# Kernel optimization log

Measured on AMD Instinct MI355X. Metric: run time of the kernel, lower is better.

## Reference

```python
import jax, jax.numpy as jnp
import numpy as np

L, B, S, CACHE = 2, 1, 2048, 2048
H, HKV, D, DM, FF, V = 16, 8, 128, 2048, 8192, 32000
EPS = 1e-6
ROPE_BASE = 10000.0


def setup_inputs() -> dict:
    key = jax.random.key(0)
    ks = jax.random.split(key, 18)
    std = 0.02
    r = lambda k, shape: (jax.random.normal(k, shape, dtype=jnp.float32) * std)
    return {
        "input_ids": jax.random.randint(ks[0], (B, S), 0, V),
        "embed": r(ks[1], (V, DM)),
        "Wq": r(ks[2], (L, DM, H * D)),
        "Wk": r(ks[3], (L, DM, HKV * D)),
        "Wv": r(ks[4], (L, DM, HKV * D)),
        "Wo": r(ks[5], (L, H * D, DM)),
        "Wg": r(ks[6], (L, DM, FF)),
        "Wu": r(ks[7], (L, DM, FF)),
        "Wd": r(ks[8], (L, FF, DM)),
        "ln1": jnp.ones((L, DM), jnp.float32),
        "ln2": jnp.ones((L, DM), jnp.float32),
        "final_norm": jnp.ones((DM,), jnp.float32),
        "lm_head": r(ks[9], (DM, V)),
        "k_cache": jax.random.normal(ks[10], (L, B, H, CACHE, D), jnp.float32),
        "v_cache": jax.random.normal(ks[11], (L, B, H, CACHE, D), jnp.float32),
    }


def rms_norm(x, w):
    return x * jax.lax.rsqrt(jnp.mean(x * x, axis=-1, keepdims=True) + EPS) * w


def apply_rope(x, pos):
    # x: [B,H,T,D], pos: [T]
    inv_freq = 1.0 / (ROPE_BASE ** (jnp.arange(0, D, 2, dtype=jnp.float32) / D))
    f = pos[:, None].astype(jnp.float32) * inv_freq[None, :]  # [T, D/2]
    emb = jnp.concatenate([f, f], axis=-1)                    # [T, D]
    cos, sin = jnp.cos(emb), jnp.sin(emb)
    rot = jnp.concatenate([-x[..., D // 2:], x[..., : D // 2]], axis=-1)
    return x * cos + rot * sin


def decoder_forward(input_ids, embed, Wq, Wk, Wv, Wo, Wg, Wu, Wd,
                    ln1, ln2, final_norm, lm_head, k_cache, v_cache):
    h = embed[input_ids]  # [B,S,DM]
    T = CACHE + S
    q_pos = jnp.arange(CACHE, CACHE + S)
    k_pos = jnp.arange(T)
    # causal mask: query i (global pos CACHE+i) attends keys <= CACHE+i
    mask = k_pos[None, :] <= (CACHE + jnp.arange(S))[:, None]  # [S,T]
    scale = 1.0 / np.sqrt(D)

    def layer(h, params):
        wq, wk, wv, wo, wg, wu, wd, l1, l2, kc, vc = params
        x = rms_norm(h, l1)
        q = (x @ wq).reshape(B, S, H, D).transpose(0, 2, 1, 3)     # [B,H,S,D]
        k = (x @ wk).reshape(B, S, HKV, D).transpose(0, 2, 1, 3)   # [B,HKV,S,D]
        v = (x @ wv).reshape(B, S, HKV, D).transpose(0, 2, 1, 3)
        k = jnp.repeat(k, H // HKV, axis=1)                        # repeat_kv
        v = jnp.repeat(v, H // HKV, axis=1)
        k = jnp.concatenate([kc, k], axis=2)                       # [B,H,T,D]
        v = jnp.concatenate([vc, v], axis=2)
        q = apply_rope(q, q_pos)
        k = apply_rope(k, k_pos)
        scores = jnp.einsum('bhqd,bhkd->bhqk', q, k) * scale
        scores = jnp.where(mask, scores, jnp.float32(-1e30))
        attn = jax.nn.softmax(scores, axis=-1)
        o = jnp.einsum('bhqk,bhkd->bhqd', attn, v)
        o = o.transpose(0, 2, 1, 3).reshape(B, S, H * D) @ wo
        h = h + o
        x = rms_norm(h, l2)
        h = h + (jax.nn.silu(x @ wg) * (x @ wu)) @ wd
        return h, None

    h, _ = jax.lax.scan(layer, h, (Wq, Wk, Wv, Wo, Wg, Wu, Wd, ln1, ln2, k_cache, v_cache))
    h = rms_norm(h, final_norm)
    return (h @ lm_head).astype(jnp.float32)  # logits [B,S,V]


def reference(input_ids, embed, Wq, Wk, Wv, Wo, Wg, Wu, Wd,
              ln1, ln2, final_norm, lm_head, k_cache, v_cache):
    return decoder_forward(input_ids, embed, Wq, Wk, Wv, Wo, Wg, Wu, Wd,
                           ln1, ln2, final_norm, lm_head, k_cache, v_cache)
```

## Files before the change

### kernel.cpp

```cpp
#include <hip/hip_runtime.h>

typedef __attribute__((ext_vector_type(8))) short bfrag8;
typedef __attribute__((ext_vector_type(4))) short bfrag4;
typedef __attribute__((ext_vector_type(4))) float facc4;

#define DEV_INLINE __device__ __forceinline__

DEV_INLINE short f2bf(float f) {
    union { float f; unsigned u; } x; x.f = f;
    unsigned r = (x.u + 0x7FFFu + ((x.u >> 16) & 1u)) >> 16;
    return (short)r;
}

DEV_INLINE unsigned pack_bf2(float a, float b) {
    return (unsigned)(unsigned short)f2bf(a) | ((unsigned)(unsigned short)f2bf(b) << 16);
}

#define GL2LDS(gp, lp) __builtin_amdgcn_global_load_lds( \
    (const __attribute__((address_space(1))) void*)(gp), \
    (__attribute__((address_space(3))) void*)(lp), 16, 0, 0)

#define MFMA16(a, b, c) __builtin_amdgcn_mfma_f32_16x16x32_bf16((a), (b), (c), 0, 0, 0)

__global__ __launch_bounds__(256) void embed_kernel(const int* __restrict__ ids,
                                                    const float* __restrict__ emb,
                                                    float* __restrict__ h) {
    int s = blockIdx.x;
    int id = ids[s];
    const float* src = emb + (size_t)id * 2048;
    float* dst = h + (size_t)s * 2048;
    int t = threadIdx.x;
    float4 a = *(const float4*)(src + t * 8);
    float4 b = *(const float4*)(src + t * 8 + 4);
    *(float4*)(dst + t * 8) = a;
    *(float4*)(dst + t * 8 + 4) = b;
}

__global__ __launch_bounds__(256) void rmsnorm_bf16_kernel(const float* __restrict__ in,
                                                           const float* __restrict__ w,
                                                           short* __restrict__ out) {
    int row = blockIdx.x;
    const float* x = in + (size_t)row * 2048;
    short* y = out + (size_t)row * 2048;
    int t = threadIdx.x;
    float4 a = *(const float4*)(x + t * 8);
    float4 b = *(const float4*)(x + t * 8 + 4);
    float ss = a.x*a.x + a.y*a.y + a.z*a.z + a.w*a.w
             + b.x*b.x + b.y*b.y + b.z*b.z + b.w*b.w;
#pragma unroll
    for (int off = 32; off >= 1; off >>= 1) ss += __shfl_xor(ss, off);
    __shared__ float red[4];
    if ((t & 63) == 0) red[t >> 6] = ss;
    __syncthreads();
    float tot = red[0] + red[1] + red[2] + red[3];
    float sc = rsqrtf(tot * (1.0f / 2048.0f) + 1e-6f);
    float4 wa = *(const float4*)(w + t * 8);
    float4 wb = *(const float4*)(w + t * 8 + 4);
    bfrag8 o;
    o[0] = f2bf(a.x * sc * wa.x); o[1] = f2bf(a.y * sc * wa.y);
    o[2] = f2bf(a.z * sc * wa.z); o[3] = f2bf(a.w * sc * wa.w);
    o[4] = f2bf(b.x * sc * wb.x); o[5] = f2bf(b.y * sc * wb.y);
    o[6] = f2bf(b.z * sc * wb.z); o[7] = f2bf(b.w * sc * wb.w);
    *(bfrag8*)(y + t * 8) = o;
}

__global__ __launch_bounds__(256) void wconv_kernel(const float* __restrict__ W,
                                                    short* __restrict__ Wt,
                                                    int K, int N) {
    __shared__ short Lt[64][72];
    int k0 = blockIdx.x * 64, n0 = blockIdx.y * 64;
    int tid = threadIdx.x;
    int r = tid >> 4, c = (tid & 15) * 4;
#pragma unroll
    for (int j = 0; j < 4; ++j) {
        int k = r + j * 16;
        float4 v = *(const float4*)(W + (size_t)(k0 + k) * N + n0 + c);
        Lt[c + 0][k] = f2bf(v.x); Lt[c + 1][k] = f2bf(v.y);
        Lt[c + 2][k] = f2bf(v.z); Lt[c + 3][k] = f2bf(v.w);
    }
    __syncthreads();
    int n = tid >> 3, kk = (tid & 7) * 8;
#pragma unroll
    for (int j = 0; j < 2; ++j)
        *(bfrag8*)(Wt + (size_t)(n0 + n + j * 32) * K + k0 + kk) = *(const bfrag8*)&Lt[n + j * 32][kk];
}

template<int BM, bool ADD>
__global__ __launch_bounds__(256) void gemm_bt(const short* __restrict__ A,
                                               const short* __restrict__ Bt,
                                               float* __restrict__ C,
                                               int K, int N) {
    __shared__ short As[BM * 32];
    __shared__ short Bs[128 * 32];
    constexpr int NW = (BM == 128) ? 4 : 2;
    int tid = threadIdx.x;
    int lane = tid & 63, wave = tid >> 6;

    int gx = gridDim.x;
    int nwg = gx * gridDim.y;
    int b = blockIdx.y * gx + blockIdx.x;
    int q = nwg >> 3, r8 = nwg & 7;
    int xcd = b & 7, idx = b >> 3;
    int lb = (xcd < r8) ? (xcd * (q + 1) + idx) : (r8 * (q + 1) + (xcd - r8) * q + idx);
    int bm = (lb % gx) * BM, bn = (lb / gx) * 128;

    int wr = (BM == 128) ? ((wave >> 1) * 64) : 0;
    int wc = (BM == 128) ? ((wave & 1) * 64) : (wave * 32);
    int lr = lane & 15, lg = lane >> 4;

    facc4 acc[4][NW];
#pragma unroll
    for (int m = 0; m < 4; ++m)
#pragma unroll
        for (int n = 0; n < NW; ++n) acc[m][n] = (facc4){0.f, 0.f, 0.f, 0.f};

    int stR = wave * 16 + (lane >> 2);
    int stK = (lane & 3) * 8;
    const short* Ag = A + (size_t)(bm + stR) * K + stK;
    const short* Bg = Bt + (size_t)(bn + stR) * K + stK;
    short* AsP = As + stR * 32 + stK;
    short* BsP = Bs + stR * 32 + stK;

    for (int k0 = 0; k0 < K; k0 += 32) {
        GL2LDS(Ag + k0, AsP);
        if (BM == 128) GL2LDS(Ag + (size_t)64 * K + k0, AsP + 64 * 32);
        GL2LDS(Bg + k0, BsP);
        GL2LDS(Bg + (size_t)64 * K + k0, BsP + 64 * 32);
        __syncthreads();
        bfrag8 a[4], bfr[NW];
#pragma unroll
        for (int m = 0; m < 4; ++m)
            a[m] = *(const bfrag8*)&As[(wr + m * 16 + lr) * 32 + lg * 8];
#pragma unroll
        for (int n = 0; n < NW; ++n)
            bfr[n] = *(const bfrag8*)&Bs[(wc + n * 16 + lr) * 32 + lg * 8];
#pragma unroll
        for (int m = 0; m < 4; ++m)
#pragma unroll
            for (int n = 0; n < NW; ++n)
                acc[m][n] = MFMA16(a[m], bfr[n], acc[m][n]);
        __syncthreads();
    }
#pragma unroll
    for (int m = 0; m < 4; ++m)
#pragma unroll
        for (int n = 0; n < NW; ++n)
#pragma unroll
            for (int r = 0; r < 4; ++r) {
                size_t ci = (size_t)(bm + wr + m * 16 + lg * 4 + r) * N + bn + wc + n * 16 + lr;
                C[ci] = ADD ? (C[ci] + acc[m][n][r]) : acc[m][n][r];
            }
}

__global__ __launch_bounds__(512, 2) void gemm8(const short* __restrict__ A,
                                                const short* __restrict__ Bt,
                                                float* __restrict__ C,
                                                int K, int N) {
    __shared__ short lds[65536];
    char* ldsb = (char*)lds;
    int tid = threadIdx.x;
    int lane = tid & 63, wave = tid >> 6;
    int wm = wave >> 2, wn = wave & 3;
    int lr = lane & 15, lg = lane >> 4;

    int gx = gridDim.x;
    int nwg = gx * gridDim.y;
    int b = blockIdx.y * gx + blockIdx.x;
    int q8 = nwg >> 3, r8 = nwg & 7;
    int xcd = b & 7, idx = b >> 3;
    int lb = (xcd < r8) ? (xcd * (q8 + 1) + idx) : (r8 * (q8 + 1) + (xcd - r8) * q8 + idx);
    int bm = (lb % gx) * 256, bn = (lb / gx) * 256;

    facc4 acc[8][4];
#pragma unroll
    for (int m = 0; m < 8; ++m)
#pragma unroll
        for (int n = 0; n < 4; ++n) acc[m][n] = (facc4){0.f, 0.f, 0.f, 0.f};

    int rs = tid >> 3;
    int swz = ((tid & 7) ^ (rs & 7)) * 8;
    int d0 = tid * 16, d1 = 8192 + tid * 16;
    const size_t sK = (size_t)K;

    auto stage = [&](int u) {
        int sp = (u & 1) * 2;
        int ko = u * 64 + swz;
        const short* Ab = A + (size_t)(bm + rs) * sK + ko;
        const short* Bb = Bt + (size_t)(bn + rs) * sK + ko;
        GL2LDS(Ab,            ldsb + sp * 16384 + d0);
        GL2LDS(Ab +  64 * sK, ldsb + sp * 16384 + d1);
        GL2LDS(Ab + 128 * sK, ldsb + (sp + 1) * 16384 + d0);
        GL2LDS(Ab + 192 * sK, ldsb + (sp + 1) * 16384 + d1);
        GL2LDS(Bb,            ldsb + 65536 + sp * 16384 + d0);
        GL2LDS(Bb +  64 * sK, ldsb + 65536 + sp * 16384 + d1);
        GL2LDS(Bb + 128 * sK, ldsb + 65536 + (sp + 1) * 16384 + d0);
        GL2LDS(Bb + 192 * sK, ldsb + 65536 + (sp + 1) * 16384 + d1);
    };

    int NT = K >> 6;
    stage(0);
    asm volatile("s_waitcnt vmcnt(0)" ::: "memory");
    __builtin_amdgcn_s_barrier();
    __builtin_amdgcn_sched_barrier(0);

    int ck0 = (lg ^ (lr & 7)) * 8;
    int aoff = lr * 64;
    int boff = ((wn & 1) * 64 + lr) * 64;

    for (int t = 0; t < NT; ++t) {
        int aA = ((t & 1) * 2 + wm) * 8192 + aoff;
        int bA = 32768 + ((t & 1) * 2 + (wn >> 1)) * 8192 + boff;
        bfrag8 af[4][2], bf[4][2];
#pragma unroll
        for (int i = 0; i < 4; ++i) {
            af[i][0] = *(const bfrag8*)&lds[aA + i * 1024 + ck0];
            af[i][1] = *(const bfrag8*)&lds[aA + i * 1024 + (ck0 ^ 32)];
        }
#pragma unroll
        for (int n = 0; n < 2; ++n) {
            bf[n][0] = *(const bfrag8*)&lds[bA + n * 1024 + ck0];
            bf[n][1] = *(const bfrag8*)&lds[bA + n * 1024 + (ck0 ^ 32)];
        }
        if (t + 1 < NT) stage(t + 1);
        __builtin_amdgcn_s_setprio(1);
#pragma unroll
        for (int i = 0; i < 4; ++i)
#pragma unroll
            for (int n = 0; n < 2; ++n) {
                acc[i][n] = MFMA16(af[i][0], bf[n][0], acc[i][n]);
                acc[i][n] = MFMA16(af[i][1], bf[n][1], acc[i][n]);
            }
        __builtin_amdgcn_s_setprio(0);
        __builtin_amdgcn_s_barrier();
        __builtin_amdgcn_sched_barrier(0);
#pragma unroll
        for (int n = 2; n < 4; ++n) {
            bf[n][0] = *(const bfrag8*)&lds[bA + n * 1024 + ck0];
            bf[n][1] = *(const bfrag8*)&lds[bA + n * 1024 + (ck0 ^ 32)];
        }
        __builtin_amdgcn_s_setprio(1);
#pragma unroll
        for (int i = 0; i < 4; ++i)
#pragma unroll
            for (int n = 2; n < 4; ++n) {
                acc[i][n] = MFMA16(af[i][0], bf[n][0], acc[i][n]);
                acc[i][n] = MFMA16(af[i][1], bf[n][1], acc[i][n]);
            }
        __builtin_amdgcn_s_setprio(0);
        __builtin_amdgcn_s_barrier();
        __builtin_amdgcn_sched_barrier(0);
#pragma unroll
        for (int i = 0; i < 4; ++i) {
            af[i][0] = *(const bfrag8*)&lds[aA + (4 + i) * 1024 + ck0];
            af[i][1] = *(const bfrag8*)&lds[aA + (4 + i) * 1024 + (ck0 ^ 32)];
        }
        __builtin_amdgcn_s_setprio(1);
#pragma unroll
        for (int i = 0; i < 4; ++i)
#pragma unroll
            for (int n = 0; n < 2; ++n) {
                acc[4 + i][n] = MFMA16(af[i][0], bf[n][0], acc[4 + i][n]);
                acc[4 + i][n] = MFMA16(af[i][1], bf[n][1], acc[4 + i][n]);
            }
        __builtin_amdgcn_s_setprio(0);
        __builtin_amdgcn_s_barrier();
        __builtin_amdgcn_sched_barrier(0);
        __builtin_amdgcn_s_setprio(1);
#pragma unroll
        for (int i = 0; i < 4; ++i)
#pragma unroll
            for (int n = 2; n < 4; ++n) {
                acc[4 + i][n] = MFMA16(af[i][0], bf[n][0], acc[4 + i][n]);
                acc[4 + i][n] = MFMA16(af[i][1], bf[n][1], acc[4 + i][n]);
            }
        __builtin_amdgcn_s_setprio(0);
        asm volatile("s_waitcnt vmcnt(0)" ::: "memory");
        __builtin_amdgcn_s_barrier();
        __builtin_amdgcn_sched_barrier(0);
    }

    int crow = bm + wm * 128 + lg * 4;
    int ccol = bn + wn * 64 + lr;
#pragma unroll
    for (int m = 0; m < 8; ++m)
#pragma unroll
        for (int n = 0; n < 4; ++n)
#pragma unroll
            for (int r = 0; r < 4; ++r)
                C[(size_t)(crow + m * 16 + r) * N + ccol + n * 16] = acc[m][n][r];
}

#define ROPE_C 0.20762050593046010f
#define INV2PI 0.15915494309189535f
#define TWOPI  6.283185307179586f
#define QK_SCALE 0.08838834764831845f

DEV_INLINE void rope_sc(float pos, int j, float* s, float* c) {
    float f = pos * exp2f(-(float)j * ROPE_C);
    float r = f * INV2PI;
    r -= floorf(r);
    __sincosf(r * TWOPI, s, c);
}

__global__ __launch_bounds__(128) void prep_q_kernel(const float* __restrict__ qkv,
                                                     short* __restrict__ Qb) {
    int h = blockIdx.x, s = blockIdx.y, d = threadIdx.x;
    const float* src = qkv + (size_t)s * 4096 + h * 128;
    float x = src[d], xp = src[d ^ 64];
    float sn, c;
    rope_sc((float)(2048 + s), d & 63, &sn, &c);
    float o = (d < 64) ? (x * c - xp * sn) : (x * c + xp * sn);
    Qb[((size_t)h * 2048 + s) * 128 + d] = f2bf(o * QK_SCALE);
}

__global__ __launch_bounds__(128) void prep_k_kernel(const float* __restrict__ kc,
                                                     const float* __restrict__ qkv,
                                                     short* __restrict__ Kf) {
    int h = blockIdx.x, t = blockIdx.y, d = threadIdx.x;
    float x, xp;
    if (t < 2048) {
        const float* src = kc + ((size_t)h * 2048 + t) * 128;
        x = src[d]; xp = src[d ^ 64];
    } else {
        const float* src = qkv + (size_t)(t - 2048) * 4096 + 2048 + (h >> 1) * 128;
        x = src[d]; xp = src[d ^ 64];
    }
    float sn, c;
    rope_sc((float)t, d & 63, &sn, &c);
    float o = (d < 64) ? (x * c - xp * sn) : (x * c + xp * sn);
    Kf[((size_t)h * 4096 + t) * 128 + d] = f2bf(o);
}

__global__ __launch_bounds__(256) void prep_v_kernel(const float* __restrict__ vc,
                                                     const float* __restrict__ qkv,
                                                     short* __restrict__ Vt) {
    int h = blockIdx.x;
    int t0 = blockIdx.y * 64;
    __shared__ short Lt[128][72];
    int tid = threadIdx.x;
    int r = tid >> 2;
    int c0 = (tid & 3) * 32;
    int t = t0 + r;
    const float* src = (t < 2048)
        ? vc + ((size_t)h * 2048 + t) * 128 + c0
        : qkv + (size_t)(t - 2048) * 4096 + 3072 + (h >> 1) * 128 + c0;
#pragma unroll
    for (int i = 0; i < 32; i += 4) {
        float4 v = *(const float4*)(src + i);
        Lt[c0 + i + 0][r] = f2bf(v.x);
        Lt[c0 + i + 1][r] = f2bf(v.y);
        Lt[c0 + i + 2][r] = f2bf(v.z);
        Lt[c0 + i + 3][r] = f2bf(v.w);
    }
    __syncthreads();
    int d = tid >> 1;
    int hh = (tid & 1) * 32;
    short* dst = Vt + ((size_t)h * 128 + d) * 4096 + t0 + hh;
    const short* srcl = &Lt[d][hh];
#pragma unroll
    for (int i = 0; i < 32; i += 8)
        *(bfrag8*)(dst + i) = *(const bfrag8*)(srcl + i);
}

__global__ __launch_bounds__(256, 4) void attn_kernel(const short* __restrict__ Q,
                                                      const short* __restrict__ Kf,
                                                      const short* __restrict__ Vt,
                                                      float* __restrict__ Op,
                                                      float* __restrict__ Ml,
                                                      float* __restrict__ Ll) {
    int h = blockIdx.x;
    int qb = blockIdx.y * 64;
    int z = blockIdx.z;
    int tid = threadIdx.x;
    int lane = tid & 63, wave = tid >> 6;
    int lr = lane & 15, lg = lane >> 4;
    int qrow = qb + wave * 16;
    int qg = 2048 + qrow + lr;

    __shared__ short Ks[2][4096];
    __shared__ short Vs[2][4096];
    __shared__ short P[4][16][40];

    const short* kbase = Kf + (size_t)h * 4096 * 128;
    const short* vbase = Vt + (size_t)h * 128 * 4096;

    bfrag8 aq[4];
    {
        const short* qp = Q + ((size_t)h * 2048 + qrow + lr) * 128 + lg * 8;
#pragma unroll
        for (int dt = 0; dt < 4; ++dt) aq[dt] = *(const bfrag8*)(qp + dt * 32);
    }
    facc4 o[8];
#pragma unroll
    for (int n = 0; n < 8; ++n) o[n] = (facc4){0.f, 0.f, 0.f, 0.f};
    float m = -1e30f, l = 0.f;

    auto stage = [&](int buf, int t0) {
#pragma unroll
        for (int half = 0; half < 2; ++half) {
            int rk = half * 16 + wave * 4 + (lane >> 4);
            int ck = (lane & 15) ^ (rk & 7);
            GL2LDS(kbase + (size_t)(t0 + rk) * 128 + ck * 8,
                   &Ks[buf][half * 2048 + wave * 512 + lane * 8]);
            int rv = half * 64 + wave * 16 + (lane >> 2);
            int cv = (lane & 3) ^ ((rv >> 1) & 3);
            GL2LDS(vbase + (size_t)rv * 4096 + t0 + cv * 8,
                   &Vs[buf][half * 2048 + wave * 512 + lane * 8]);
        }
    };

    auto process = [&](int buf, int t0) {
        facc4 s0 = (facc4){0.f, 0.f, 0.f, 0.f}, s1 = (facc4){0.f, 0.f, 0.f, 0.f};
        int r0 = lr, r1 = 16 + lr;
#pragma unroll
        for (int dt = 0; dt < 4; ++dt) {
            bfrag8 k0 = *(const bfrag8*)&Ks[buf][r0 * 128 + (((dt * 4 + lg) ^ (r0 & 7)) * 8)];
            bfrag8 k1 = *(const bfrag8*)&Ks[buf][r1 * 128 + (((dt * 4 + lg) ^ (r1 & 7)) * 8)];
            s0 = MFMA16(k0, aq[dt], s0);
            s1 = MFMA16(k1, aq[dt], s1);
        }
        float mx = m;
#pragma unroll
        for (int r = 0; r < 4; ++r) {
            int k0i = t0 + lg * 4 + r;
            if (k0i > qg)      s0[r] = -1e30f;
            if (k0i + 16 > qg) s1[r] = -1e30f;
            mx = fmaxf(mx, fmaxf(s0[r], s1[r]));
        }
        mx = fmaxf(mx, __shfl_xor(mx, 16));
        mx = fmaxf(mx, __shfl_xor(mx, 32));
        if (__any(mx > m + 8.f)) {
            float alpha = __expf(m - mx);
            m = mx;
            l *= alpha;
            float ab[4];
#pragma unroll
            for (int r = 0; r < 4; ++r) ab[r] = __shfl(alpha, lg * 4 + r);
#pragma unroll
            for (int n = 0; n < 8; ++n) {
                o[n][0] *= ab[0]; o[n][1] *= ab[1]; o[n][2] *= ab[2]; o[n][3] *= ab[3];
            }
        }
        float ps = 0.f;
#pragma unroll
        for (int r = 0; r < 4; ++r) {
            s0[r] = __expf(s0[r] - m); ps += s0[r];
            s1[r] = __expf(s1[r] - m); ps += s1[r];
        }
        ps += __shfl_xor(ps, 16);
        ps += __shfl_xor(ps, 32);
        l += ps;
        unsigned* prow = (unsigned*)&P[wave][lr][0];
        prow[lg * 2]     = pack_bf2(s0[0], s0[1]);
        prow[lg * 2 + 1] = pack_bf2(s0[2], s0[3]);
        prow[8 + lg * 2]     = pack_bf2(s1[0], s1[1]);
        prow[8 + lg * 2 + 1] = pack_bf2(s1[2], s1[3]);
        bfrag8 ap = *(const bfrag8*)&P[wave][lr][lg * 8];
#pragma unroll
        for (int n = 0; n < 8; ++n) {
            int rv = n * 16 + lr;
            bfrag8 vf = *(const bfrag8*)&Vs[buf][rv * 32 + ((lg ^ ((rv >> 1) & 3)) * 8)];
            o[n] = MFMA16(ap, vf, o[n]);
        }
    };

    int NT = ((2048 + qb + 63) >> 5) + 1;
    int i0 = z ? (NT >> 1) : 0;
    int i1 = z ? NT : (NT >> 1);

    stage(0, i0 * 32);
    __syncthreads();
    int buf = 0;
    for (int i = i0; i < i1; ++i) {
        if (i + 1 < i1) stage(buf ^ 1, (i + 1) * 32);
        process(buf, i * 32);
        __syncthreads();
        buf ^= 1;
    }

#pragma unroll
    for (int n = 0; n < 8; ++n)
#pragma unroll
        for (int r = 0; r < 4; ++r)
            Op[(size_t)(z * 2048 + qrow + lg * 4 + r) * 2048 + h * 128 + n * 16 + lr] = o[n][r];
    if (lg == 0) {
        Ml[((size_t)z * 16 + h) * 2048 + qrow + lr] = m;
        Ll[((size_t)z * 16 + h) * 2048 + qrow + lr] = l;
    }
}

__global__ __launch_bounds__(256) void attn_combine(const float* __restrict__ Op,
                                                    const float* __restrict__ Ml,
                                                    const float* __restrict__ Ll,
                                                    short* __restrict__ Ob) {
    int row = blockIdx.x, t = threadIdx.x;
    int col0 = t * 8;
    int h = col0 >> 7;
    float m0 = Ml[(size_t)h * 2048 + row], m1 = Ml[(size_t)(16 + h) * 2048 + row];
    float l0 = Ll[(size_t)h * 2048 + row], l1 = Ll[(size_t)(16 + h) * 2048 + row];
    float mm = fmaxf(m0, m1);
    float a0 = __expf(m0 - mm), a1 = __expf(m1 - mm);
    float inv = 1.f / (l0 * a0 + l1 * a1);
    a0 *= inv; a1 *= inv;
    const float* p0 = Op + (size_t)row * 2048 + col0;
    const float* p1 = Op + (size_t)(2048 + row) * 2048 + col0;
    float4 x0 = *(const float4*)p0, x1 = *(const float4*)(p0 + 4);
    float4 y0 = *(const float4*)p1, y1 = *(const float4*)(p1 + 4);
    bfrag8 ov;
    ov[0] = f2bf(x0.x * a0 + y0.x * a1); ov[1] = f2bf(x0.y * a0 + y0.y * a1);
    ov[2] = f2bf(x0.z * a0 + y0.z * a1); ov[3] = f2bf(x0.w * a0 + y0.w * a1);
    ov[4] = f2bf(x1.x * a0 + y1.x * a1); ov[5] = f2bf(x1.y * a0 + y1.y * a1);
    ov[6] = f2bf(x1.z * a0 + y1.z * a1); ov[7] = f2bf(x1.w * a0 + y1.w * a1);
    *(bfrag8*)(Ob + (size_t)row * 2048 + col0) = ov;
}

__global__ __launch_bounds__(256) void silu_mul_bf16_kernel(const float* __restrict__ g,
                                                            const float* __restrict__ u,
                                                            short* __restrict__ out) {
    size_t i = ((size_t)blockIdx.x * 256 + threadIdx.x) * 4;
    float4 x = *(const float4*)(g + i);
    float4 y = *(const float4*)(u + i);
    bfrag4 o;
    o[0] = f2bf(x.x / (1.f + __expf(-x.x)) * y.x);
    o[1] = f2bf(x.y / (1.f + __expf(-x.y)) * y.y);
    o[2] = f2bf(x.z / (1.f + __expf(-x.z)) * y.z);
    o[3] = f2bf(x.w / (1.f + __expf(-x.w)) * y.w);
    *(bfrag4*)(out + i) = o;
}

extern "C" void kernel_launch(void* const* d_in, const int* in_sizes, int n_in,
                              void* d_out, int out_size, void* d_ws, size_t ws_size,
                              hipStream_t stream) {
    const int*   ids   = (const int*)d_in[0];
    const float* emb   = (const float*)d_in[1];
    const float* Wq    = (const float*)d_in[2];
    const float* Wk    = (const float*)d_in[3];
    const float* Wv    = (const float*)d_in[4];
    const float* Wo    = (const float*)d_in[5];
    const float* Wg    = (const float*)d_in[6];
    const float* Wu    = (const float*)d_in[7];
    const float* Wd    = (const float*)d_in[8];
    const float* ln1   = (const float*)d_in[9];
    const float* ln2   = (const float*)d_in[10];
    const float* fnorm = (const float*)d_in[11];
    const float* lmh   = (const float*)d_in[12];
    const float* kc    = (const float*)d_in[13];
    const float* vc    = (const float*)d_in[14];
    float* logits = (float*)d_out;

    char* ws = (char*)d_ws;
    float* hbuf   = (float*)(ws + ((size_t)0 << 20));
    short* xb     = (short*)(ws + ((size_t)16 << 20));
    float* qkvbuf = (float*)(ws + ((size_t)24 << 20));
    short* Ob     = (short*)(ws + ((size_t)56 << 20));
    short* wt     = (short*)(ws + ((size_t)64 << 20));
    short* Qb     = (short*)(ws + ((size_t)98 << 20));
    short* Kf     = (short*)(ws + ((size_t)106 << 20));
    short* Vt     = (short*)(ws + ((size_t)122 << 20));
    float* gbuf   = (float*)(ws + ((size_t)138 << 20));
    float* ubuf   = (float*)(ws + ((size_t)202 << 20));
    short* gb     = (short*)(ws + ((size_t)266 << 20));
    float* mlb    = (float*)(ws + ((size_t)298 << 20));
    float* Mlp    = mlb;
    float* Llp    = mlb + 2 * 16 * 2048;
    short* lmwt   = (short*)(ws + ((size_t)138 << 20));

    embed_kernel<<<2048, 256, 0, stream>>>(ids, emb, hbuf);

    for (int l = 0; l < 2; ++l) {
        const float* wq  = Wq + (size_t)l * 2048 * 2048;
        const float* wk  = Wk + (size_t)l * 2048 * 1024;
        const float* wv  = Wv + (size_t)l * 2048 * 1024;
        const float* wo  = Wo + (size_t)l * 2048 * 2048;
        const float* wg  = Wg + (size_t)l * 2048 * 8192;
        const float* wu  = Wu + (size_t)l * 2048 * 8192;
        const float* wd  = Wd + (size_t)l * 8192 * 2048;
        const float* l1  = ln1 + (size_t)l * 2048;
        const float* l2  = ln2 + (size_t)l * 2048;
        const float* kcl = kc + (size_t)l * 16 * 2048 * 128;
        const float* vcl = vc + (size_t)l * 16 * 2048 * 128;

        rmsnorm_bf16_kernel<<<2048, 256, 0, stream>>>(hbuf, l1, xb);
        wconv_kernel<<<dim3(32, 32), 256, 0, stream>>>(wq, wt, 2048, 2048);
        wconv_kernel<<<dim3(32, 16), 256, 0, stream>>>(wk, wt + (size_t)2048 * 2048, 2048, 1024);
        wconv_kernel<<<dim3(32, 16), 256, 0, stream>>>(wv, wt + (size_t)3072 * 2048, 2048, 1024);
        gemm_bt<128, false><<<dim3(16, 32), 256, 0, stream>>>(xb, wt, qkvbuf, 2048, 4096);
        prep_q_kernel<<<dim3(16, 2048), 128, 0, stream>>>(qkvbuf, Qb);
        prep_k_kernel<<<dim3(16, 4096), 128, 0, stream>>>(kcl, qkvbuf, Kf);
        prep_v_kernel<<<dim3(16, 64), 256, 0, stream>>>(vcl, qkvbuf, Vt);
        attn_kernel<<<dim3(16, 32, 2), 256, 0, stream>>>(Qb, Kf, Vt, qkvbuf, Mlp, Llp);
        attn_combine<<<2048, 256, 0, stream>>>(qkvbuf, Mlp, Llp, Ob);
        wconv_kernel<<<dim3(32, 32), 256, 0, stream>>>(wo, wt, 2048, 2048);
        gemm_bt<64, true><<<dim3(32, 16), 256, 0, stream>>>(Ob, wt, hbuf, 2048, 2048);
        rmsnorm_bf16_kernel<<<2048, 256, 0, stream>>>(hbuf, l2, xb);
        wconv_kernel<<<dim3(32, 128), 256, 0, stream>>>(wg, wt, 2048, 8192);
        gemm8<<<dim3(8, 32), 512, 0, stream>>>(xb, wt, gbuf, 2048, 8192);
        wconv_kernel<<<dim3(32, 128), 256, 0, stream>>>(wu, wt, 2048, 8192);
        gemm8<<<dim3(8, 32), 512, 0, stream>>>(xb, wt, ubuf, 2048, 8192);
        silu_mul_bf16_kernel<<<16384, 256, 0, stream>>>(gbuf, ubuf, gb);
        wconv_kernel<<<dim3(128, 32), 256, 0, stream>>>(wd, wt, 8192, 2048);
        gemm_bt<64, true><<<dim3(32, 16), 256, 0, stream>>>(gb, wt, hbuf, 8192, 2048);
    }
    rmsnorm_bf16_kernel<<<2048, 256, 0, stream>>>(hbuf, fnorm, xb);
    wconv_kernel<<<dim3(32, 500), 256, 0, stream>>>(lmh, lmwt, 2048, 32000);
    gemm8<<<dim3(8, 125), 512, 0, stream>>>(xb, lmwt, logits, 2048, 32000);
}
```

Before: 1.743 ms.

## Retile gemm8 to 256x128 with three-stage LDS pipeline and reuse for QKV

```diff
diff --git a/kernel.cpp b/kernel.cpp
--- a/kernel.cpp
+++ b/kernel.cpp
@@ -152,15 +152,15 @@
             }
 }
 
-__global__ __launch_bounds__(512, 2) void gemm8(const short* __restrict__ A,
+__global__ __launch_bounds__(512, 1) void gemm8(const short* __restrict__ A,
                                                 const short* __restrict__ Bt,
                                                 float* __restrict__ C,
                                                 int K, int N) {
-    __shared__ short lds[65536];
+    __shared__ short lds[73728];
     char* ldsb = (char*)lds;
     int tid = threadIdx.x;
     int lane = tid & 63, wave = tid >> 6;
-    int wm = wave >> 2, wn = wave & 3;
+    int wm = wave >> 1, wn = wave & 1;
     int lr = lane & 15, lg = lane >> 4;
 
     int gx = gridDim.x;
@@ -169,120 +169,99 @@
     int q8 = nwg >> 3, r8 = nwg & 7;
     int xcd = b & 7, idx = b >> 3;
     int lb = (xcd < r8) ? (xcd * (q8 + 1) + idx) : (r8 * (q8 + 1) + (xcd - r8) * q8 + idx);
-    int bm = (lb % gx) * 256, bn = (lb / gx) * 256;
-
-    facc4 acc[8][4];
-#pragma unroll
-    for (int m = 0; m < 8; ++m)
+    int bm = (lb % gx) * 256, bn = (lb / gx) * 128;
+
+    facc4 acc[4][4];
+#pragma unroll
+    for (int m = 0; m < 4; ++m)
 #pragma unroll
         for (int n = 0; n < 4; ++n) acc[m][n] = (facc4){0.f, 0.f, 0.f, 0.f};
 
     int rs = tid >> 3;
     int swz = ((tid & 7) ^ (rs & 7)) * 8;
-    int d0 = tid * 16, d1 = 8192 + tid * 16;
     const size_t sK = (size_t)K;
+    const short* Abase = A + (size_t)(bm + rs) * sK + swz;
+    const short* Bbase = Bt + (size_t)(bn + rs) * sK + swz;
 
     auto stage = [&](int u) {
-        int sp = (u & 1) * 2;
-        int ko = u * 64 + swz;
-        const short* Ab = A + (size_t)(bm + rs) * sK + ko;
-        const short* Bb = Bt + (size_t)(bn + rs) * sK + ko;
-        GL2LDS(Ab,            ldsb + sp * 16384 + d0);
-        GL2LDS(Ab +  64 * sK, ldsb + sp * 16384 + d1);
-        GL2LDS(Ab + 128 * sK, ldsb + (sp + 1) * 16384 + d0);
-        GL2LDS(Ab + 192 * sK, ldsb + (sp + 1) * 16384 + d1);
-        GL2LDS(Bb,            ldsb + 65536 + sp * 16384 + d0);
-        GL2LDS(Bb +  64 * sK, ldsb + 65536 + sp * 16384 + d1);
-        GL2LDS(Bb + 128 * sK, ldsb + 65536 + (sp + 1) * 16384 + d0);
-        GL2LDS(Bb + 192 * sK, ldsb + 65536 + (sp + 1) * 16384 + d1);
+        int sl = u % 3;
+        int ko = u * 64;
+        const short* Ab = Abase + ko;
+        const short* Bb = Bbase + ko;
+        char* Ad = ldsb + sl * 32768 + tid * 16;
+        char* Bd = ldsb + 98304 + sl * 16384 + tid * 16;
+        GL2LDS(Ab,            Ad);
+        GL2LDS(Ab +  64 * sK, Ad + 8192);
+        GL2LDS(Ab + 128 * sK, Ad + 16384);
+        GL2LDS(Ab + 192 * sK, Ad + 24576);
+        GL2LDS(Bb,            Bd);
+        GL2LDS(Bb +  64 * sK, Bd + 8192);
     };
 
     int NT = K >> 6;
     stage(0);
-    asm volatile("s_waitcnt vmcnt(0)" ::: "memory");
+    stage(1);
+    asm volatile("s_waitcnt vmcnt(6)" ::: "memory");
     __builtin_amdgcn_s_barrier();
     __builtin_amdgcn_sched_barrier(0);
 
-    int ck0 = (lg ^ (lr & 7)) * 8;
-    int aoff = lr * 64;
-    int boff = ((wn & 1) * 64 + lr) * 64;
-
     for (int t = 0; t < NT; ++t) {
-        int aA = ((t & 1) * 2 + wm) * 8192 + aoff;
-        int bA = 32768 + ((t & 1) * 2 + (wn >> 1)) * 8192 + boff;
+        int sl = t % 3;
+        const short* As_ = lds + sl * 16384;
+        const short* Bs_ = lds + 49152 + sl * 8192;
         bfrag8 af[4][2], bf[4][2];
 #pragma unroll
-        for (int i = 0; i < 4; ++i) {
-            af[i][0] = *(const bfrag8*)&lds[aA + i * 1024 + ck0];
-            af[i][1] = *(const bfrag8*)&lds[aA + i * 1024 + (ck0 ^ 32)];
+        for (int m = 0; m < 4; ++m) {
+            int row = wm * 64 + m * 16 + lr;
+#pragma unroll
+            for (int kk = 0; kk < 2; ++kk)
+                af[m][kk] = *(const bfrag8*)&As_[row * 64 + (((kk * 4 + lg) ^ (row & 7)) * 8)];
         }
 #pragma unroll
         for (int n = 0; n < 2; ++n) {
-            bf[n][0] = *(const bfrag8*)&lds[bA + n * 1024 + ck0];
-            bf[n][1] = *(const bfrag8*)&lds[bA + n * 1024 + (ck0 ^ 32)];
-        }
-        if (t + 1 < NT) stage(t + 1);
+            int row = wn * 64 + n * 16 + lr;
+#pragma unroll
+            for (int kk = 0; kk < 2; ++kk)
+                bf[n][kk] = *(const bfrag8*)&Bs_[row * 64 + (((kk * 4 + lg) ^ (row & 7)) * 8)];
+        }
+        if (t + 2 < NT) stage(t + 2);
         __builtin_amdgcn_s_setprio(1);
 #pragma unroll
-        for (int i = 0; i < 4; ++i)
+        for (int m = 0; m < 4; ++m)
 #pragma unroll
             for (int n = 0; n < 2; ++n) {
-                acc[i][n] = MFMA16(af[i][0], bf[n][0], acc[i][n]);
-                acc[i][n] = MFMA16(af[i][1], bf[n][1], acc[i][n]);
+                acc[m][n] = MFMA16(af[m][0], bf[n][0], acc[m][n]);
+                acc[m][n] = MFMA16(af[m][1], bf[n][1], acc[m][n]);
             }
         __builtin_amdgcn_s_setprio(0);
-        __builtin_amdgcn_s_barrier();
-        __builtin_amdgcn_sched_barrier(0);
 #pragma unroll
         for (int n = 2; n < 4; ++n) {
-            bf[n][0] = *(const bfrag8*)&lds[bA + n * 1024 + ck0];
-            bf[n][1] = *(const bfrag8*)&lds[bA + n * 1024 + (ck0 ^ 32)];
+            int row = wn * 64 + n * 16 + lr;
+#pragma unroll
+            for (int kk = 0; kk < 2; ++kk)
+                bf[n][kk] = *(const bfrag8*)&Bs_[row * 64 + (((kk * 4 + lg) ^ (row & 7)) * 8)];
         }
         __builtin_amdgcn_s_setprio(1);
 #pragma unroll
-        for (int i = 0; i < 4; ++i)
+        for (int m = 0; m < 4; ++m)
 #pragma unroll
             for (int n = 2; n < 4; ++n) {
-                acc[i][n] = MFMA16(af[i][0], bf[n][0], acc[i][n]);
-                acc[i][n] = MFMA16(af[i][1], bf[n][1], acc[i][n]);
+                acc[m][n] = MFMA16(af[m][0], bf[n][0], acc[m][n]);
+                acc[m][n] = MFMA16(af[m][1], bf[n][1], acc[m][n]);
             }
         __builtin_amdgcn_s_setprio(0);
-        __builtin_amdgcn_s_barrier();
-        __builtin_amdgcn_sched_barrier(0);
-#pragma unroll
-        for (int i = 0; i < 4; ++i) {
-            af[i][0] = *(const bfrag8*)&lds[aA + (4 + i) * 1024 + ck0];
-            af[i][1] = *(const bfrag8*)&lds[aA + (4 + i) * 1024 + (ck0 ^ 32)];
-        }
-        __builtin_amdgcn_s_setprio(1);
-#pragma unroll
-        for (int i = 0; i < 4; ++i)
-#pragma unroll
-            for (int n = 0; n < 2; ++n) {
-                acc[4 + i][n] = MFMA16(af[i][0], bf[n][0], acc[4 + i][n]);
-                acc[4 + i][n] = MFMA16(af[i][1], bf[n][1], acc[4 + i][n]);
-            }
-        __builtin_amdgcn_s_setprio(0);
-        __builtin_amdgcn_s_barrier();
-        __builtin_amdgcn_sched_barrier(0);
-        __builtin_amdgcn_s_setprio(1);
-#pragma unroll
-        for (int i = 0; i < 4; ++i)
-#pragma unroll
-            for (int n = 2; n < 4; ++n) {
-                acc[4 + i][n] = MFMA16(af[i][0], bf[n][0], acc[4 + i][n]);
-                acc[4 + i][n] = MFMA16(af[i][1], bf[n][1], acc[4 + i][n]);
-            }
-        __builtin_amdgcn_s_setprio(0);
-        asm volatile("s_waitcnt vmcnt(0)" ::: "memory");
-        __builtin_amdgcn_s_barrier();
-        __builtin_amdgcn_sched_barrier(0);
-    }
-
-    int crow = bm + wm * 128 + lg * 4;
+        if (t + 1 < NT) {
+            if (t + 2 < NT) asm volatile("s_waitcnt vmcnt(6)" ::: "memory");
+            else            asm volatile("s_waitcnt vmcnt(0)" ::: "memory");
+            __builtin_amdgcn_s_barrier();
+            __builtin_amdgcn_sched_barrier(0);
+        }
+    }
+
+    int crow = bm + wm * 64 + lg * 4;
     int ccol = bn + wn * 64 + lr;
 #pragma unroll
-    for (int m = 0; m < 8; ++m)
+    for (int m = 0; m < 4; ++m)
 #pragma unroll
         for (int n = 0; n < 4; ++n)
 #pragma unroll
@@ -584,7 +563,7 @@
         wconv_kernel<<<dim3(32, 32), 256, 0, stream>>>(wq, wt, 2048, 2048);
         wconv_kernel<<<dim3(32, 16), 256, 0, stream>>>(wk, wt + (size_t)2048 * 2048, 2048, 1024);
         wconv_kernel<<<dim3(32, 16), 256, 0, stream>>>(wv, wt + (size_t)3072 * 2048, 2048, 1024);
-        gemm_bt<128, false><<<dim3(16, 32), 256, 0, stream>>>(xb, wt, qkvbuf, 2048, 4096);
+        gemm8<<<dim3(8, 32), 512, 0, stream>>>(xb, wt, qkvbuf, 2048, 4096);
         prep_q_kernel<<<dim3(16, 2048), 128, 0, stream>>>(qkvbuf, Qb);
         prep_k_kernel<<<dim3(16, 4096), 128, 0, stream>>>(kcl, qkvbuf, Kf);
         prep_v_kernel<<<dim3(16, 64), 256, 0, stream>>>(vcl, qkvbuf, Vt);
@@ -594,14 +573,14 @@
         gemm_bt<64, true><<<dim3(32, 16), 256, 0, stream>>>(Ob, wt, hbuf, 2048, 2048);
         rmsnorm_bf16_kernel<<<2048, 256, 0, stream>>>(hbuf, l2, xb);
         wconv_kernel<<<dim3(32, 128), 256, 0, stream>>>(wg, wt, 2048, 8192);
-        gemm8<<<dim3(8, 32), 512, 0, stream>>>(xb, wt, gbuf, 2048, 8192);
+        gemm8<<<dim3(8, 64), 512, 0, stream>>>(xb, wt, gbuf, 2048, 8192);
         wconv_kernel<<<dim3(32, 128), 256, 0, stream>>>(wu, wt, 2048, 8192);
-        gemm8<<<dim3(8, 32), 512, 0, stream>>>(xb, wt, ubuf, 2048, 8192);
+        gemm8<<<dim3(8, 64), 512, 0, stream>>>(xb, wt, ubuf, 2048, 8192);
         silu_mul_bf16_kernel<<<16384, 256, 0, stream>>>(gbuf, ubuf, gb);
         wconv_kernel<<<dim3(128, 32), 256, 0, stream>>>(wd, wt, 8192, 2048);
         gemm_bt<64, true><<<dim3(32, 16), 256, 0, stream>>>(gb, wt, hbuf, 8192, 2048);
     }
     rmsnorm_bf16_kernel<<<2048, 256, 0, stream>>>(hbuf, fnorm, xb);
     wconv_kernel<<<dim3(32, 500), 256, 0, stream>>>(lmh, lmwt, 2048, 32000);
-    gemm8<<<dim3(8, 125), 512, 0, stream>>>(xb, lmwt, logits, 2048, 32000);
-}
+    gemm8<<<dim3(8, 250), 512, 0, stream>>>(xb, lmwt, logits, 2048, 32000);
+}
```

Result: slower. 1.796 ms (+3.1%).
